# Kernel tuning notes

Hardware: AMD Instinct MI355X
Metric: run time of the kernel (lower is better)

Reference implementation:

```python
import jax, jax.numpy as jnp
import numpy as np

NUM_GROUPS = 32
EPS = 1e-5


def setup_inputs() -> dict:
    key = jax.random.key(0)
    ks = jax.random.split(key, 4)
    B, C, H, W = 4, 256, 64, 64
    x = jax.random.normal(ks[0], (B, C, H, W), dtype=jnp.float32)
    norm_w = jnp.ones((C,), dtype=jnp.float32)
    norm_b = jnp.zeros((C,), dtype=jnp.float32)
    qkv_w = jax.random.normal(ks[1], (3 * C, C), dtype=jnp.float32) * (C ** -0.5)
    qkv_b = jnp.zeros((3 * C,), dtype=jnp.float32)
    proj_w = jax.random.normal(ks[2], (C, C), dtype=jnp.float32) * (C ** -0.5)
    proj_b = jnp.zeros((C,), dtype=jnp.float32)
    return {"x": x, "norm_w": norm_w, "norm_b": norm_b, "qkv_w": qkv_w,
            "qkv_b": qkv_b, "proj_w": proj_w, "proj_b": proj_b, "num_heads": 1}


def _group_norm(x, w, b):
    B, C, H, W = x.shape
    xg = x.reshape(B, NUM_GROUPS, C // NUM_GROUPS, H, W)
    mean = xg.mean(axis=(2, 3, 4), keepdims=True)
    var = xg.var(axis=(2, 3, 4), keepdims=True)
    xn = ((xg - mean) * jax.lax.rsqrt(var + EPS)).reshape(B, C, H, W)
    return xn * w[None, :, None, None] + b[None, :, None, None]


def reference(x, norm_w, norm_b, qkv_w, qkv_b, proj_w, proj_b, num_heads):
    B, C, H, W = x.shape
    N = H * W
    d = C // num_heads
    xn = _group_norm(x, norm_w, norm_b)
    # 1x1 conv == channel matmul: [B,3C,H,W]
    qkv = jnp.einsum('oc,bchw->bohw', qkv_w, xn) + qkv_b[None, :, None, None]
    qkv = qkv.reshape(B, 3, num_heads, d, N)
    q, k, v = qkv[:, 0], qkv[:, 1], qkv[:, 2]  # each [B,h,d,N]
    scale = d ** -0.5
    attn = jnp.einsum('bhdi,bhdj->bhij', q, k) * scale  # [B,h,N,N]
    attn = jax.nn.softmax(attn, axis=-1)
    out = jnp.einsum('bhij,bhdj->bhdi', attn, v)  # [B,h,d,N]
    out = out.reshape(B, C, H, W)
    out = jnp.einsum('oc,bchw->bohw', proj_w, out) + proj_b[None, :, None, None]
    return x + out
```

## Files before the change

kernel.cpp:

```cpp
#include <hip/hip_runtime.h>
#include <stdint.h>
#include <stddef.h>

#define NB 4
#define NC 256
#define NSP 4096
#define NG 32
#define CPG 8
#define GEPS 1e-5f
#define SCALE 0.0625f
#define NROWS (NB * NSP)
#define JSPLIT 4

typedef __attribute__((ext_vector_type(8))) short s8v;
typedef __attribute__((ext_vector_type(4))) float f4v;
typedef __attribute__((ext_vector_type(4))) unsigned short us4v;

__device__ __forceinline__ float b2f(unsigned short h) {
  union { unsigned u; float f; } x; x.u = ((unsigned)h) << 16; return x.f;
}
__device__ __forceinline__ unsigned short f2b(float f) {
  union { float f; unsigned u; } x; x.f = f;
  unsigned r = x.u + 0x7fffu + ((x.u >> 16) & 1u);
  return (unsigned short)(r >> 16);
}

__global__ __launch_bounds__(256) void cvt_kernel(const float* __restrict__ in,
                                                  unsigned short* __restrict__ out, int n) {
  int i = (blockIdx.x * 256 + threadIdx.x) * 4;
  if (i < n) {
    float4 v = *(const float4*)(in + i);
    us4v p;
    p[0] = f2b(v.x); p[1] = f2b(v.y); p[2] = f2b(v.z); p[3] = f2b(v.w);
    *(us4v*)(out + i) = p;
  }
}

__global__ __launch_bounds__(256) void gn_kernel(
    const float* __restrict__ x, const float* __restrict__ w,
    const float* __restrict__ bias, unsigned short* __restrict__ xn) {
  int b = blockIdx.x >> 5;
  int g = blockIdx.x & 31;
  const float* xp = x + ((size_t)b * NC + (size_t)g * CPG) * NSP;
  int t = threadIdx.x;
  float s = 0.f, ss = 0.f;
  for (int i = 4 * t; i < CPG * NSP; i += 1024) {
    float4 v = *(const float4*)(xp + i);
    s += v.x + v.y + v.z + v.w;
    ss += v.x * v.x + v.y * v.y + v.z * v.z + v.w * v.w;
  }
  __shared__ float r1[256], r2[256];
  r1[t] = s; r2[t] = ss;
  __syncthreads();
  for (int off = 128; off > 0; off >>= 1) {
    if (t < off) { r1[t] += r1[t + off]; r2[t] += r2[t + off]; }
    __syncthreads();
  }
  float mean = r1[0] * (1.f / (CPG * NSP));
  float var  = r2[0] * (1.f / (CPG * NSP)) - mean * mean;
  float rstd = rsqrtf(var + GEPS);
  float wv[CPG], bv[CPG];
  for (int c = 0; c < CPG; c++) {
    wv[c] = w[g * CPG + c] * rstd;
    bv[c] = bias[g * CPG + c] - mean * wv[c];
  }
  for (int n = t; n < NSP; n += 256) {
    s8v pk;
    for (int c = 0; c < CPG; c++) {
      float v = xp[(size_t)c * NSP + n];
      ((unsigned short*)&pk)[c] = f2b(v * wv[c] + bv[c]);
    }
    *(s8v*)(xn + ((size_t)(b * NSP + n) * NC + g * CPG)) = pk;
  }
}

template<int MODE, int HAS_BIAS, int HAS_RES>
__global__ __launch_bounds__(256) void gemm_nt(
    const unsigned short* __restrict__ A, const unsigned short* __restrict__ Bt,
    void* __restrict__ Cv, const float* __restrict__ bias,
    const float* __restrict__ res,
    int M, int N, int K, int ldC, float scale,
    long long sA, long long sB, long long sC, long long sR) {
  A  += (size_t)blockIdx.z * sA;
  Bt += (size_t)blockIdx.z * sB;
  if (HAS_RES) res += (size_t)blockIdx.z * sR;
  const int m0 = blockIdx.y * 128, n0 = blockIdx.x * 128;
  __shared__ unsigned short As[128 * 32], Bs[128 * 32];
  const int t = threadIdx.x;
  const int lane = t & 63, wave = t >> 6;
  const int wm = (wave >> 1) * 64, wn = (wave & 1) * 64;
  const int l16 = lane & 15, quad = lane >> 4;
  const int srow = t >> 2, skc = (t & 3) * 8;

  f4v acc[4][4];
  for (int mi = 0; mi < 4; mi++)
    for (int ni = 0; ni < 4; ni++)
      acc[mi][ni] = (f4v){0.f, 0.f, 0.f, 0.f};

  const unsigned short* Ag0 = A  + (size_t)(m0 + srow) * K + skc;
  const unsigned short* Ag1 = A  + (size_t)(m0 + srow + 64) * K + skc;
  const unsigned short* Bg0 = Bt + (size_t)(n0 + srow) * K + skc;
  const unsigned short* Bg1 = Bt + (size_t)(n0 + srow + 64) * K + skc;

  for (int k0 = 0; k0 < K; k0 += 32) {
    s8v a0 = *(const s8v*)(Ag0 + k0);
    s8v a1 = *(const s8v*)(Ag1 + k0);
    s8v b0 = *(const s8v*)(Bg0 + k0);
    s8v b1 = *(const s8v*)(Bg1 + k0);
    __syncthreads();
    *(s8v*)(As + srow * 32 + skc) = a0;
    *(s8v*)(As + (srow + 64) * 32 + skc) = a1;
    *(s8v*)(Bs + srow * 32 + skc) = b0;
    *(s8v*)(Bs + (srow + 64) * 32 + skc) = b1;
    __syncthreads();
    s8v af[4], bfr[4];
    for (int mi = 0; mi < 4; mi++)
      af[mi] = *(const s8v*)(As + (wm + mi * 16 + l16) * 32 + quad * 8);
    for (int ni = 0; ni < 4; ni++)
      bfr[ni] = *(const s8v*)(Bs + (wn + ni * 16 + l16) * 32 + quad * 8);
    for (int mi = 0; mi < 4; mi++)
      for (int ni = 0; ni < 4; ni++)
        acc[mi][ni] = __builtin_amdgcn_mfma_f32_16x16x32_bf16(af[mi], bfr[ni], acc[mi][ni], 0, 0, 0);
  }

  for (int mi = 0; mi < 4; mi++) {
    const int rb = m0 + wm + mi * 16 + quad * 4;
    for (int ni = 0; ni < 4; ni++) {
      const int col = n0 + wn + ni * 16 + l16;
      f4v a = acc[mi][ni];
      if (MODE == 3) {
        float* C = (float*)Cv + (size_t)blockIdx.z * sC;
        for (int r = 0; r < 4; r++) {
          float v = a[r] * scale;
          if (HAS_BIAS) v += bias[rb + r];
          if (HAS_RES) v += res[(size_t)(rb + r) * ldC + col];
          C[(size_t)(rb + r) * ldC + col] = v;
        }
      } else if (MODE == 1) {
        unsigned short* C = (unsigned short*)Cv + (size_t)blockIdx.z * sC;
        us4v pk;
        for (int r = 0; r < 4; r++) {
          float v = a[r] * scale;
          if (HAS_BIAS) v += bias[rb + r];
          pk[r] = (unsigned short)f2b(v);
        }
        const size_t off = ((size_t)((col >> 4) * 8 + (rb >> 5))) * 512 +
                           (((rb >> 3) & 3) * 16 + (col & 15)) * 8 + (rb & 7);
        *(us4v*)(C + off) = pk;
      } else if (MODE == 2) {
        unsigned short* C = (unsigned short*)Cv + (size_t)blockIdx.z * sC;
        for (int r = 0; r < 4; r++) {
          float v = a[r] * scale;
          if (HAS_BIAS) v += bias[rb + r];
          const int d = rb + r;
          const size_t off = ((size_t)((col >> 5) * 16 + (d >> 4))) * 512 +
                             (((col >> 3) & 3) * 16 + (d & 15)) * 8 + (col & 7);
          C[off] = f2b(v);
        }
      } else {
        unsigned short* C = (unsigned short*)Cv + (size_t)blockIdx.z * sC;
        for (int r = 0; r < 4; r++) {
          float v = a[r] * scale;
          if (HAS_BIAS) v += bias[rb + r];
          if (HAS_RES) v += res[(size_t)(rb + r) * ldC + col];
          C[(size_t)(rb + r) * ldC + col] = f2b(v);
        }
      }
    }
  }
}

__global__ __launch_bounds__(256, 2) void flash5_kernel(
    const unsigned short* __restrict__ q, const unsigned short* __restrict__ k,
    const unsigned short* __restrict__ v, unsigned short* __restrict__ Opart,
    float* __restrict__ Lpart) {
  const int qt = blockIdx.x, b = blockIdx.y, js = blockIdx.z;
  const size_t sNC = (size_t)NSP * NC;
  const unsigned short* qb = q + b * sNC;
  const unsigned short* kb = k + b * sNC;
  const unsigned short* vb = v + b * sNC;
  const int t = threadIdx.x, lane = t & 63, w = t >> 6;
  const int l16 = lane & 15, quad = lane >> 4;

  __shared__ unsigned short KfLds[2][16 * 512];
  __shared__ unsigned short VfLds[2][16 * 512];
  __shared__ unsigned short Ps[4][2][16 * 40];

  s8v qf[2][8];
  for (int f = 0; f < 2; f++)
    for (int kc = 0; kc < 8; kc++)
      qf[f][kc] = *(const s8v*)(qb + (size_t)((qt * 8 + f * 4 + w) * 8 + kc) * 512 + lane * 8);

  f4v accO[2][16];
  for (int f = 0; f < 2; f++)
    for (int dt = 0; dt < 16; dt++) accO[f][dt] = (f4v){0.f, 0.f, 0.f, 0.f};
  float l_acc[2][4];
  for (int f = 0; f < 2; f++)
    for (int r = 0; r < 4; r++) l_acc[f][r] = 0.f;

  const int jbeg = js * (NSP / JSPLIT);
  const int NT = (NSP / JSPLIT) / 32;

  auto stage = [&](int j0, int bufsel) {
    unsigned short* Kd = KfLds[bufsel];
    unsigned short* Vd = VfLds[bufsel];
    for (int ii = 0; ii < 8; ii++) {
      const int idx = w * 8 + ii;
      if (idx < 16) {
        const unsigned short* gp =
            kb + (size_t)(((j0 >> 4) + (idx >> 3)) * 8 + (idx & 7)) * 512 + lane * 8;
        __builtin_amdgcn_global_load_lds(
            (const __attribute__((address_space(1))) unsigned int*)gp,
            (__attribute__((address_space(3))) unsigned int*)(Kd + idx * 512),
            16, 0, 0);
      } else {
        const int dt = idx - 16;
        const unsigned short* gp =
            vb + (size_t)((j0 >> 5) * 16 + dt) * 512 + lane * 8;
        __builtin_amdgcn_global_load_lds(
            (const __attribute__((address_space(1))) unsigned int*)gp,
            (__attribute__((address_space(3))) unsigned int*)(Vd + dt * 512),
            16, 0, 0);
      }
    }
  };

  stage(jbeg, 0);
  for (int jt = 0; jt < NT; jt++) {
    __syncthreads();
    if (jt + 1 < NT) stage(jbeg + (jt + 1) * 32, (jt + 1) & 1);
    const unsigned short* Kc = KfLds[jt & 1];
    const unsigned short* Vc = VfLds[jt & 1];

    f4v accS[2][2];
    for (int f = 0; f < 2; f++)
      for (int n = 0; n < 2; n++) accS[f][n] = (f4v){0.f, 0.f, 0.f, 0.f};
    for (int kc = 0; kc < 8; kc++) {
      s8v kf0 = *(const s8v*)(Kc + kc * 512 + lane * 8);
      s8v kf1 = *(const s8v*)(Kc + (8 + kc) * 512 + lane * 8);
      for (int f = 0; f < 2; f++) {
        accS[f][0] = __builtin_amdgcn_mfma_f32_16x16x32_bf16(qf[f][kc], kf0, accS[f][0], 0, 0, 0);
        accS[f][1] = __builtin_amdgcn_mfma_f32_16x16x32_bf16(qf[f][kc], kf1, accS[f][1], 0, 0, 0);
      }
    }

    for (int f = 0; f < 2; f++) {
      for (int n = 0; n < 2; n++)
        for (int r = 0; r < 4; r++) {
          const float pv = __expf(accS[f][n][r] * SCALE);
          accS[f][n][r] = pv;
          l_acc[f][r] += pv;
        }
      for (int n = 0; n < 2; n++)
        for (int r = 0; r < 4; r++)
          Ps[w][f][(quad * 4 + r) * 40 + n * 16 + l16] = f2b(accS[f][n][r]);
    }
    s8v pf0 = *(const s8v*)(&Ps[w][0][0] + l16 * 40 + quad * 8);
    s8v pf1 = *(const s8v*)(&Ps[w][1][0] + l16 * 40 + quad * 8);

    for (int dt = 0; dt < 16; dt++) {
      s8v vf = *(const s8v*)(Vc + dt * 512 + lane * 8);
      accO[0][dt] = __builtin_amdgcn_mfma_f32_16x16x32_bf16(pf0, vf, accO[0][dt], 0, 0, 0);
      accO[1][dt] = __builtin_amdgcn_mfma_f32_16x16x32_bf16(pf1, vf, accO[1][dt], 0, 0, 0);
    }
  }

  for (int f = 0; f < 2; f++) {
    const int ibase = qt * 128 + f * 64 + w * 16;
    const int prow = b * NSP + ibase;
    unsigned short* Op = Opart + ((size_t)js * NROWS + prow) * NC;
    for (int dt = 0; dt < 16; dt++)
      for (int r = 0; r < 4; r++)
        Op[(size_t)(quad * 4 + r) * NC + dt * 16 + l16] = f2b(accO[f][dt][r]);
    for (int r = 0; r < 4; r++) {
      float lv = l_acc[f][r];
      lv += __shfl_xor(lv, 1, 64);
      lv += __shfl_xor(lv, 2, 64);
      lv += __shfl_xor(lv, 4, 64);
      lv += __shfl_xor(lv, 8, 64);
      if (l16 == 0) Lpart[(size_t)js * NROWS + prow + quad * 4 + r] = lv;
    }
  }
}

__global__ __launch_bounds__(256) void merge_kernel(
    const unsigned short* __restrict__ Opart, const float* __restrict__ Lpart,
    unsigned short* __restrict__ at) {
  const int t = threadIdx.x;
  const int row = blockIdx.x * 4 + (t >> 6);
  const int d0 = (t & 63) * 4;
  float lsum = 0.f;
  for (int js = 0; js < JSPLIT; js++) lsum += Lpart[(size_t)js * NROWS + row];
  const float inv = 1.f / lsum;
  float acc[4] = {0.f, 0.f, 0.f, 0.f};
  for (int js = 0; js < JSPLIT; js++) {
    us4v o = *(const us4v*)(Opart + ((size_t)js * NROWS + row) * NC + d0);
    for (int i = 0; i < 4; i++) acc[i] += b2f(o[i]);
  }
  us4v pk;
  for (int i = 0; i < 4; i++) pk[i] = f2b(acc[i] * inv);
  *(us4v*)(at + (size_t)row * NC + d0) = pk;
}

extern "C" void kernel_launch(void* const* d_in, const int* in_sizes, int n_in,
                              void* d_out, int out_size, void* d_ws, size_t ws_size,
                              hipStream_t stream) {
  const float* x      = (const float*)d_in[0];
  const float* norm_w = (const float*)d_in[1];
  const float* norm_b = (const float*)d_in[2];
  const float* qkv_w  = (const float*)d_in[3];
  const float* qkv_b  = (const float*)d_in[4];
  const float* proj_w = (const float*)d_in[5];
  const float* proj_b = (const float*)d_in[6];
  float* out = (float*)d_out;

  char* ws = (char*)d_ws;
  unsigned short* wq = (unsigned short*)ws;
  unsigned short* wp = (unsigned short*)(ws + 3 * NC * NC * 2);
  char* wst = ws + (1 << 20);
  const size_t szBNC = (size_t)NB * NSP * NC * 2;
  unsigned short* xn = (unsigned short*)wst;
  unsigned short* q  = (unsigned short*)(wst + szBNC);
  unsigned short* k  = (unsigned short*)(wst + 2 * szBNC);
  unsigned short* v  = (unsigned short*)(wst + 3 * szBNC);
  unsigned short* at = xn;
  unsigned short* Opart = (unsigned short*)(wst + 4 * szBNC);
  float* Lpart = (float*)(wst + 4 * szBNC + (size_t)JSPLIT * NROWS * NC * 2);

  cvt_kernel<<<dim3(3 * NC * NC / 1024), 256, 0, stream>>>(qkv_w, wq, 3 * NC * NC);
  cvt_kernel<<<dim3(NC * NC / 1024), 256, 0, stream>>>(proj_w, wp, NC * NC);
  gn_kernel<<<dim3(NB * NG), 256, 0, stream>>>(x, norm_w, norm_b, xn);

  const long long sNC = (long long)NSP * NC;
  gemm_nt<1, 1, 0><<<dim3(NSP / 128, NC / 128, NB), 256, 0, stream>>>(
      wq, xn, q, qkv_b, nullptr, NC, NSP, NC, NC, 1.f, 0, sNC, sNC, 0);
  gemm_nt<1, 1, 0><<<dim3(NSP / 128, NC / 128, NB), 256, 0, stream>>>(
      wq + NC * NC, xn, k, qkv_b + NC, nullptr, NC, NSP, NC, NC, 1.f, 0, sNC, sNC, 0);
  gemm_nt<2, 1, 0><<<dim3(NSP / 128, NC / 128, NB), 256, 0, stream>>>(
      wq + 2 * NC * NC, xn, v, qkv_b + 2 * NC, nullptr, NC, NSP, NC, NSP, 1.f, 0, sNC, sNC, 0);

  flash5_kernel<<<dim3(NSP / 128, NB, JSPLIT), 256, 0, stream>>>(q, k, v, Opart, Lpart);
  merge_kernel<<<dim3(NROWS / 4), 256, 0, stream>>>(Opart, Lpart, at);

  gemm_nt<3, 1, 1><<<dim3(NSP / 128, NC / 128, NB), 256, 0, stream>>>(
      wp, at, out, proj_b, x, NC, NSP, NC, NSP, 1.f, 0, sNC, sNC, sNC);
}
```

Baseline: 227.6 us.

## Fuse QKV GEMMs, fold merge into projection GEMM, prescale Q

```diff
diff --git a/kernel.cpp b/kernel.cpp
--- a/kernel.cpp
+++ b/kernel.cpp
@@ -24,16 +24,22 @@
   unsigned r = x.u + 0x7fffu + ((x.u >> 16) & 1u);
   return (unsigned short)(r >> 16);
 }
-
-__global__ __launch_bounds__(256) void cvt_kernel(const float* __restrict__ in,
-                                                  unsigned short* __restrict__ out, int n) {
+__device__ __forceinline__ unsigned short f2b_rtz(float f) {
+  union { float f; unsigned u; } x; x.f = f;
+  return (unsigned short)(x.u >> 16);
+}
+
+__global__ __launch_bounds__(256) void cvt2_kernel(
+    const float* __restrict__ qw, const float* __restrict__ pw,
+    unsigned short* __restrict__ wq, unsigned short* __restrict__ wp) {
   int i = (blockIdx.x * 256 + threadIdx.x) * 4;
-  if (i < n) {
-    float4 v = *(const float4*)(in + i);
-    us4v p;
-    p[0] = f2b(v.x); p[1] = f2b(v.y); p[2] = f2b(v.z); p[3] = f2b(v.w);
-    *(us4v*)(out + i) = p;
-  }
+  const float* src; unsigned short* dst; int j;
+  if (i < 3 * NC * NC) { src = qw; dst = wq; j = i; }
+  else { src = pw; dst = wp; j = i - 3 * NC * NC; }
+  float4 v = *(const float4*)(src + j);
+  us4v p;
+  p[0] = f2b(v.x); p[1] = f2b(v.y); p[2] = f2b(v.z); p[3] = f2b(v.w);
+  *(us4v*)(dst + j) = p;
 }
 
 __global__ __launch_bounds__(256) void gn_kernel(
@@ -74,17 +80,19 @@
   }
 }
 
-template<int MODE, int HAS_BIAS, int HAS_RES>
-__global__ __launch_bounds__(256) void gemm_nt(
-    const unsigned short* __restrict__ A, const unsigned short* __restrict__ Bt,
-    void* __restrict__ Cv, const float* __restrict__ bias,
-    const float* __restrict__ res,
-    int M, int N, int K, int ldC, float scale,
-    long long sA, long long sB, long long sC, long long sR) {
-  A  += (size_t)blockIdx.z * sA;
-  Bt += (size_t)blockIdx.z * sB;
-  if (HAS_RES) res += (size_t)blockIdx.z * sR;
-  const int m0 = blockIdx.y * 128, n0 = blockIdx.x * 128;
+__global__ __launch_bounds__(256) void qkv_gemm(
+    const unsigned short* __restrict__ W, const unsigned short* __restrict__ xnG,
+    const float* __restrict__ qkvb,
+    unsigned short* __restrict__ q, unsigned short* __restrict__ k,
+    unsigned short* __restrict__ v) {
+  const int sec = blockIdx.y >> 1;
+  const int m0 = (blockIdx.y & 1) * 128;
+  const int n0 = blockIdx.x * 128;
+  const unsigned short* A  = W + (size_t)sec * NC * NC;
+  const unsigned short* Bt = xnG + (size_t)blockIdx.z * NSP * NC;
+  unsigned short* dst = (sec == 0 ? q : (sec == 1 ? k : v)) + (size_t)blockIdx.z * NSP * NC;
+  const float scl = (sec == 0) ? SCALE : 1.f;
+
   __shared__ unsigned short As[128 * 32], Bs[128 * 32];
   const int t = threadIdx.x;
   const int lane = t & 63, wave = t >> 6;
@@ -97,12 +105,12 @@
     for (int ni = 0; ni < 4; ni++)
       acc[mi][ni] = (f4v){0.f, 0.f, 0.f, 0.f};
 
-  const unsigned short* Ag0 = A  + (size_t)(m0 + srow) * K + skc;
-  const unsigned short* Ag1 = A  + (size_t)(m0 + srow + 64) * K + skc;
-  const unsigned short* Bg0 = Bt + (size_t)(n0 + srow) * K + skc;
-  const unsigned short* Bg1 = Bt + (size_t)(n0 + srow + 64) * K + skc;
-
-  for (int k0 = 0; k0 < K; k0 += 32) {
+  const unsigned short* Ag0 = A  + (size_t)(m0 + srow) * NC + skc;
+  const unsigned short* Ag1 = A  + (size_t)(m0 + srow + 64) * NC + skc;
+  const unsigned short* Bg0 = Bt + (size_t)(n0 + srow) * NC + skc;
+  const unsigned short* Bg1 = Bt + (size_t)(n0 + srow + 64) * NC + skc;
+
+  for (int k0 = 0; k0 < NC; k0 += 32) {
     s8v a0 = *(const s8v*)(Ag0 + k0);
     s8v a1 = *(const s8v*)(Ag1 + k0);
     s8v b0 = *(const s8v*)(Bg0 + k0);
@@ -128,42 +136,19 @@
     for (int ni = 0; ni < 4; ni++) {
       const int col = n0 + wn + ni * 16 + l16;
       f4v a = acc[mi][ni];
-      if (MODE == 3) {
-        float* C = (float*)Cv + (size_t)blockIdx.z * sC;
-        for (int r = 0; r < 4; r++) {
-          float v = a[r] * scale;
-          if (HAS_BIAS) v += bias[rb + r];
-          if (HAS_RES) v += res[(size_t)(rb + r) * ldC + col];
-          C[(size_t)(rb + r) * ldC + col] = v;
-        }
-      } else if (MODE == 1) {
-        unsigned short* C = (unsigned short*)Cv + (size_t)blockIdx.z * sC;
+      if (sec < 2) {
         us4v pk;
-        for (int r = 0; r < 4; r++) {
-          float v = a[r] * scale;
-          if (HAS_BIAS) v += bias[rb + r];
-          pk[r] = (unsigned short)f2b(v);
-        }
+        for (int r = 0; r < 4; r++)
+          pk[r] = (unsigned short)f2b((a[r] + qkvb[sec * NC + rb + r]) * scl);
         const size_t off = ((size_t)((col >> 4) * 8 + (rb >> 5))) * 512 +
                            (((rb >> 3) & 3) * 16 + (col & 15)) * 8 + (rb & 7);
-        *(us4v*)(C + off) = pk;
-      } else if (MODE == 2) {
-        unsigned short* C = (unsigned short*)Cv + (size_t)blockIdx.z * sC;
+        *(us4v*)(dst + off) = pk;
+      } else {
         for (int r = 0; r < 4; r++) {
-          float v = a[r] * scale;
-          if (HAS_BIAS) v += bias[rb + r];
           const int d = rb + r;
           const size_t off = ((size_t)((col >> 5) * 16 + (d >> 4))) * 512 +
                              (((col >> 3) & 3) * 16 + (d & 15)) * 8 + (col & 7);
-          C[off] = f2b(v);
-        }
-      } else {
-        unsigned short* C = (unsigned short*)Cv + (size_t)blockIdx.z * sC;
-        for (int r = 0; r < 4; r++) {
-          float v = a[r] * scale;
-          if (HAS_BIAS) v += bias[rb + r];
-          if (HAS_RES) v += res[(size_t)(rb + r) * ldC + col];
-          C[(size_t)(rb + r) * ldC + col] = f2b(v);
+          dst[off] = f2b(a[r] + qkvb[2 * NC + d]);
         }
       }
     }
@@ -247,13 +232,13 @@
     for (int f = 0; f < 2; f++) {
       for (int n = 0; n < 2; n++)
         for (int r = 0; r < 4; r++) {
-          const float pv = __expf(accS[f][n][r] * SCALE);
+          const float pv = __expf(accS[f][n][r]);
           accS[f][n][r] = pv;
           l_acc[f][r] += pv;
         }
       for (int n = 0; n < 2; n++)
         for (int r = 0; r < 4; r++)
-          Ps[w][f][(quad * 4 + r) * 40 + n * 16 + l16] = f2b(accS[f][n][r]);
+          Ps[w][f][(quad * 4 + r) * 40 + n * 16 + l16] = f2b_rtz(accS[f][n][r]);
     }
     s8v pf0 = *(const s8v*)(&Ps[w][0][0] + l16 * 40 + quad * 8);
     s8v pf1 = *(const s8v*)(&Ps[w][1][0] + l16 * 40 + quad * 8);
@@ -283,23 +268,81 @@
   }
 }
 
-__global__ __launch_bounds__(256) void merge_kernel(
-    const unsigned short* __restrict__ Opart, const float* __restrict__ Lpart,
-    unsigned short* __restrict__ at) {
+__global__ __launch_bounds__(256) void proj_gemm(
+    const unsigned short* __restrict__ Wp, const unsigned short* __restrict__ Opart,
+    const float* __restrict__ Lpart, const float* __restrict__ pb,
+    const float* __restrict__ x, float* __restrict__ out) {
+  const int z = blockIdx.z, m0 = blockIdx.y * 128, n0 = blockIdx.x * 128;
+  __shared__ unsigned short As[128 * 32], Bs[128 * 32];
   const int t = threadIdx.x;
-  const int row = blockIdx.x * 4 + (t >> 6);
-  const int d0 = (t & 63) * 4;
-  float lsum = 0.f;
-  for (int js = 0; js < JSPLIT; js++) lsum += Lpart[(size_t)js * NROWS + row];
-  const float inv = 1.f / lsum;
-  float acc[4] = {0.f, 0.f, 0.f, 0.f};
+  const int lane = t & 63, wave = t >> 6;
+  const int wm = (wave >> 1) * 64, wn = (wave & 1) * 64;
+  const int l16 = lane & 15, quad = lane >> 4;
+  const int srow = t >> 2, skc = (t & 3) * 8;
+
+  const int prow0 = z * NSP + n0 + srow;
+  const int prow1 = prow0 + 64;
+  float ls0 = 0.f, ls1 = 0.f;
   for (int js = 0; js < JSPLIT; js++) {
-    us4v o = *(const us4v*)(Opart + ((size_t)js * NROWS + row) * NC + d0);
-    for (int i = 0; i < 4; i++) acc[i] += b2f(o[i]);
-  }
-  us4v pk;
-  for (int i = 0; i < 4; i++) pk[i] = f2b(acc[i] * inv);
-  *(us4v*)(at + (size_t)row * NC + d0) = pk;
+    ls0 += Lpart[(size_t)js * NROWS + prow0];
+    ls1 += Lpart[(size_t)js * NROWS + prow1];
+  }
+  const float inv0 = 1.f / ls0, inv1 = 1.f / ls1;
+
+  f4v acc[4][4];
+  for (int mi = 0; mi < 4; mi++)
+    for (int ni = 0; ni < 4; ni++)
+      acc[mi][ni] = (f4v){0.f, 0.f, 0.f, 0.f};
+
+  const unsigned short* Ag0 = Wp + (size_t)(m0 + srow) * NC + skc;
+  const unsigned short* Ag1 = Wp + (size_t)(m0 + srow + 64) * NC + skc;
+
+  for (int k0 = 0; k0 < NC; k0 += 32) {
+    s8v a0 = *(const s8v*)(Ag0 + k0);
+    s8v a1 = *(const s8v*)(Ag1 + k0);
+    float bv0[8], bv1[8];
+    for (int e = 0; e < 8; e++) { bv0[e] = 0.f; bv1[e] = 0.f; }
+    for (int js = 0; js < JSPLIT; js++) {
+      const s8v o0 = *(const s8v*)(Opart + ((size_t)js * NROWS + prow0) * NC + k0 + skc);
+      const s8v o1 = *(const s8v*)(Opart + ((size_t)js * NROWS + prow1) * NC + k0 + skc);
+      for (int e = 0; e < 8; e++) {
+        bv0[e] += b2f(((const unsigned short*)&o0)[e]);
+        bv1[e] += b2f(((const unsigned short*)&o1)[e]);
+      }
+    }
+    s8v b0, b1;
+    for (int e = 0; e < 8; e++) {
+      ((unsigned short*)&b0)[e] = f2b(bv0[e] * inv0);
+      ((unsigned short*)&b1)[e] = f2b(bv1[e] * inv1);
+    }
+    __syncthreads();
+    *(s8v*)(As + srow * 32 + skc) = a0;
+    *(s8v*)(As + (srow + 64) * 32 + skc) = a1;
+    *(s8v*)(Bs + srow * 32 + skc) = b0;
+    *(s8v*)(Bs + (srow + 64) * 32 + skc) = b1;
+    __syncthreads();
+    s8v af[4], bfr[4];
+    for (int mi = 0; mi < 4; mi++)
+      af[mi] = *(const s8v*)(As + (wm + mi * 16 + l16) * 32 + quad * 8);
+    for (int ni = 0; ni < 4; ni++)
+      bfr[ni] = *(const s8v*)(Bs + (wn + ni * 16 + l16) * 32 + quad * 8);
+    for (int mi = 0; mi < 4; mi++)
+      for (int ni = 0; ni < 4; ni++)
+        acc[mi][ni] = __builtin_amdgcn_mfma_f32_16x16x32_bf16(af[mi], bfr[ni], acc[mi][ni], 0, 0, 0);
+  }
+
+  float* C = out + (size_t)z * NC * NSP;
+  const float* R = x + (size_t)z * NC * NSP;
+  for (int mi = 0; mi < 4; mi++) {
+    const int rb = m0 + wm + mi * 16 + quad * 4;
+    for (int ni = 0; ni < 4; ni++) {
+      const int col = n0 + wn + ni * 16 + l16;
+      f4v a = acc[mi][ni];
+      for (int r = 0; r < 4; r++)
+        C[(size_t)(rb + r) * NSP + col] =
+            a[r] + pb[rb + r] + R[(size_t)(rb + r) * NSP + col];
+    }
+  }
 }
 
 extern "C" void kernel_launch(void* const* d_in, const int* in_sizes, int n_in,
@@ -323,25 +366,13 @@
   unsigned short* q  = (unsigned short*)(wst + szBNC);
   unsigned short* k  = (unsigned short*)(wst + 2 * szBNC);
   unsigned short* v  = (unsigned short*)(wst + 3 * szBNC);
-  unsigned short* at = xn;
   unsigned short* Opart = (unsigned short*)(wst + 4 * szBNC);
   float* Lpart = (float*)(wst + 4 * szBNC + (size_t)JSPLIT * NROWS * NC * 2);
 
-  cvt_kernel<<<dim3(3 * NC * NC / 1024), 256, 0, stream>>>(qkv_w, wq, 3 * NC * NC);
-  cvt_kernel<<<dim3(NC * NC / 1024), 256, 0, stream>>>(proj_w, wp, NC * NC);
+  cvt2_kernel<<<dim3(4 * NC * NC / 1024), 256, 0, stream>>>(qkv_w, proj_w, wq, wp);
   gn_kernel<<<dim3(NB * NG), 256, 0, stream>>>(x, norm_w, norm_b, xn);
-
-  const long long sNC = (long long)NSP * NC;
-  gemm_nt<1, 1, 0><<<dim3(NSP / 128, NC / 128, NB), 256, 0, stream>>>(
-      wq, xn, q, qkv_b, nullptr, NC, NSP, NC, NC, 1.f, 0, sNC, sNC, 0);
-  gemm_nt<1, 1, 0><<<dim3(NSP / 128, NC / 128, NB), 256, 0, stream>>>(
-      wq + NC * NC, xn, k, qkv_b + NC, nullptr, NC, NSP, NC, NC, 1.f, 0, sNC, sNC, 0);
-  gemm_nt<2, 1, 0><<<dim3(NSP / 128, NC / 128, NB), 256, 0, stream>>>(
-      wq + 2 * NC * NC, xn, v, qkv_b + 2 * NC, nullptr, NC, NSP, NC, NSP, 1.f, 0, sNC, sNC, 0);
-
+  qkv_gemm<<<dim3(NSP / 128, 6, NB), 256, 0, stream>>>(wq, xn, qkv_b, q, k, v);
   flash5_kernel<<<dim3(NSP / 128, NB, JSPLIT), 256, 0, stream>>>(q, k, v, Opart, Lpart);
-  merge_kernel<<<dim3(NROWS / 4), 256, 0, stream>>>(Opart, Lpart, at);
-
-  gemm_nt<3, 1, 1><<<dim3(NSP / 128, NC / 128, NB), 256, 0, stream>>>(
-      wp, at, out, proj_b, x, NC, NSP, NC, NSP, 1.f, 0, sNC, sNC, sNC);
-}
+  proj_gemm<<<dim3(NSP / 128, NC / 128, NB), 256, 0, stream>>>(
+      wp, Opart, Lpart, proj_b, x, out);
+}
```

After: 211.2 us. -7.2%, faster.
